# Kernel tuning notes

Hardware: AMD Instinct MI355X
Metric: run time of the kernel (lower is better)

Reference implementation:

```python
import jax, jax.numpy as jnp
from jax import lax
import numpy as np

B, C_IN, H, W = 4, 64, 192, 192
NPT = 128          # num_point
MAXC = 32          # objects per image
INIT_STRIDE, COARSE_STRIDE, DOWN = 10.0, 4.0, 4.0


def setup_inputs() -> dict:
    key = jax.random.key(0)
    ks = jax.random.split(key, 8)
    wh_pred = jax.random.normal(ks[0], (B, 2 * NPT, H, W), jnp.float32)
    cnn_feature = jax.random.normal(ks[1], (B, C_IN, H, W), jnp.float32)
    conv1_w = jax.random.normal(ks[2], (256, C_IN, 3, 3), jnp.float32) * 0.05
    conv1_b = jnp.zeros((256,), jnp.float32)
    conv2_w = jax.random.normal(ks[3], (C_IN, 256, 1, 1), jnp.float32) * 0.05
    conv2_b = jnp.zeros((C_IN,), jnp.float32)
    w_poly = jax.random.normal(ks[4], (NPT * 4, (NPT + 1) * C_IN), jnp.float32) * 0.02
    w_fuse = jax.random.normal(ks[5], (NPT * 2, NPT * 4), jnp.float32) * 0.02
    b_fuse = jnp.zeros((NPT * 2,), jnp.float32)
    ct_ind = jax.random.randint(ks[6], (B, MAXC), 0, H * W, jnp.int32)
    ct_img_idx = jnp.repeat(jnp.arange(B, dtype=jnp.int32), MAXC).reshape(B, MAXC)
    ct_num = jnp.full((B,), MAXC, jnp.int32)
    return {"wh_pred": wh_pred, "cnn_feature": cnn_feature,
            "conv1_w": conv1_w, "conv1_b": conv1_b, "conv2_w": conv2_w, "conv2_b": conv2_b,
            "w_poly": w_poly, "w_fuse": w_fuse, "b_fuse": b_fuse,
            "ct_ind": ct_ind, "ct_img_idx": ct_img_idx, "ct_num": ct_num}


def _conv(x, w, b, pad):
    y = lax.conv_general_dilated(x, w, (1, 1), [(pad, pad), (pad, pad)],
                                 dimension_numbers=("NCHW", "OIHW", "NCHW"))
    return y + b[None, :, None, None]


def _pnp(polys, h, w):
    # even-odd ray-casting rasterization: polys [N,P,2] (x,y) -> masks [N,h,w]
    N, P, _ = polys.shape
    yy = jnp.arange(h, dtype=polys.dtype)[None, :, None]   # [1,h,1]
    xx = jnp.arange(w, dtype=polys.dtype)[None, None, :]   # [1,1,w]
    v2 = jnp.roll(polys, -1, axis=1)
    edges = (polys[:, :, 0].T, polys[:, :, 1].T, v2[:, :, 0].T, v2[:, :, 1].T)  # each [P,N]

    def step(par, e):
        x1, y1, x2, y2 = [a[:, None, None] for a in e]      # [N,1,1]
        cond = (y1 > yy) != (y2 > yy)
        den = y2 - y1
        den = jnp.where(jnp.abs(den) < 1e-9, 1e-9, den)
        xint = x1 + (x2 - x1) * (yy - y1) / den
        return jnp.logical_xor(par, cond & (xx < xint)), None

    par0 = jnp.zeros((N, h, w), dtype=bool)
    par, _ = lax.scan(step, par0, edges)
    return par.astype(polys.dtype)


def _mask_batch(mask, ct_num, bs, h, w):
    # faithful to original buggy scatter: offset uses ct_num[i-1], not a cumulative sum
    cn = [int(v) for v in np.asarray(ct_num)]
    mc = max(cn)
    mb = jnp.zeros((bs, mc, h, w), mask.dtype)
    mb = mb.at[0, :cn[0]].set(mask[:cn[0]])
    for i in range(1, bs):
        mb = mb.at[i, :cn[i]].set(mask[cn[i - 1]:cn[i - 1] + cn[i]])
    return mb


def _sample(feat, pts, img_idx):
    # bilinear grid_sample (align_corners=False, zero padding): feat [B,C,H,W], pts [N,P,2] pixel coords
    Bf, C, Hf, Wf = feat.shape
    x = pts[..., 0] - 0.5
    y = pts[..., 1] - 0.5
    x0f = jnp.floor(x); y0f = jnp.floor(y)
    wx = (x - x0f)[..., None]; wy = (y - y0f)[..., None]
    x0 = x0f.astype(jnp.int32); y0 = y0f.astype(jnp.int32)

    def g(xi, yi):
        valid = (xi >= 0) & (xi < Wf) & (yi >= 0) & (yi < Hf)
        v = feat[img_idx[:, None], :, jnp.clip(yi, 0, Hf - 1), jnp.clip(xi, 0, Wf - 1)]  # [N,P,C]
        return v * valid[..., None]

    out = (g(x0, y0) * (1 - wx) * (1 - wy) + g(x0 + 1, y0) * wx * (1 - wy)
           + g(x0, y0 + 1) * (1 - wx) * wy + g(x0 + 1, y0 + 1) * wx * wy)
    return jnp.transpose(out, (0, 2, 1))  # [N,C,P]


def _decode(wh_pred, cnn_feature, conv1_w, conv1_b, conv2_w, conv2_b,
            w_poly, w_fuse, b_fuse, ct_ind, ct_img_idx, ct_num):
    bs, _, h, w = cnn_feature.shape
    ind = ct_ind.reshape(-1)        # ct_01 assumed all valid
    img = ct_img_idx.reshape(-1)
    cx = ind % w
    cy = ind // w
    off = wh_pred[img, :, cy, cx].reshape(ind.shape[0], -1, 2)   # [N, num_point, 2]
    ct = jnp.stack([cx, cy], axis=1).astype(wh_pred.dtype)       # [N,2]
    init_polys = off * INIT_STRIDE + ct[:, None, :]

    # Refine_wtih_pnp.trans_feature
    t = jax.nn.relu(_conv(cnn_feature, conv1_w, conv1_b, 1))
    feat = _conv(t, conv2_w, conv2_b, 0)

    # PnP_contour_feature (init)
    m_init = _pnp(init_polys, h, w)
    mb_init = _mask_batch(m_init, ct_num, bs, h, w)
    feat = jax.nn.relu(jnp.max(mb_init, axis=1, keepdims=True) * feat + feat)

    # GCN-style point feature sampling + global deform
    pts = jnp.concatenate([ct[:, None, :], init_polys], axis=1)  # [N, P+1, 2]
    fp = _sample(feat, pts, img).reshape(ind.shape[0], -1)       # [N, C*(P+1)]
    offsets = ((fp @ w_poly.T) @ w_fuse.T + b_fuse).reshape(-1, NPT, 2)
    coarse = offsets * COARSE_STRIDE + lax.stop_gradient(init_polys)

    # coarse_pnp
    m_c = _pnp(coarse, h, w)
    mb_c = _mask_batch(m_c, ct_num, bs, h, w)
    feat = jax.nn.relu(jnp.max(mb_c, axis=1, keepdims=True) * feat + feat)

    return init_polys * DOWN, coarse * DOWN, mb_init, mb_c, feat


def reference(wh_pred, cnn_feature, conv1_w, conv1_b, conv2_w, conv2_b,
              w_poly, w_fuse, b_fuse, ct_ind, ct_img_idx, ct_num):
    return _decode(wh_pred, cnn_feature, conv1_w, conv1_b, conv2_w, conv2_b,
                   w_poly, w_fuse, b_fuse, ct_ind, ct_img_idx, ct_num)
```

## Files before the change

kernel.cpp:

```cpp
#include <hip/hip_runtime.h>
#include <hip/hip_bf16.h>

#define HH 192
#define WW 192
#define HW 36864
#define CHW 2359296

typedef __attribute__((ext_vector_type(8))) short short8;
typedef __attribute__((ext_vector_type(4))) float float4v;

static __device__ __forceinline__ unsigned short f2bu(float f) {
  union { float f; unsigned u; } v; v.f = f;
  unsigned r = (v.u + 0x7fffu + ((v.u >> 16) & 1u)) >> 16;
  return (unsigned short)r;
}

static __device__ __forceinline__ float bu2f(unsigned short s) {
  union { unsigned u; float f; } v; v.u = ((unsigned)s) << 16;
  return v.f;
}

__global__ void k_prep(const float* __restrict__ c1w, const float* __restrict__ c2w,
                       const float* __restrict__ wfuse,
                       unsigned short* __restrict__ wB1, unsigned short* __restrict__ wB2,
                       float* __restrict__ wfT, float* __restrict__ tmp) {
  int i = blockIdx.x * 256 + threadIdx.x;
  if (i < 147456) {
    int T = i / 9216, r = i % 9216;
    int s = r / 512, e = r % 512;
    int l = e >> 3, j = e & 7;
    int m = l & 15, q = l >> 4;
    int oc = T * 16 + m;
    int k = s * 32 + q * 8 + j;
    int tap = k >> 6, ic = k & 63;
    int ky = tap / 3, kx = tap % 3;
    wB1[i] = f2bu(c1w[((oc * 64 + ic) * 3 + ky) * 3 + kx]);
    return;
  }
  int j2 = i - 147456;
  if (j2 < 16384) {
    int g = j2 / 512, e = j2 % 512;
    int l = e >> 3, jj = e & 7;
    int m = l & 15, q = l >> 4;
    int w = g / 8, s2 = g % 8;
    wB2[j2] = f2bu(c2w[(w * 16 + m) * 256 + s2 * 32 + q * 8 + jj]);
    return;
  }
  int k3 = j2 - 16384;
  if (k3 < 131072) { int jj = k3 >> 8, r = k3 & 255; wfT[k3] = wfuse[r * 512 + jj]; return; }
  int z = k3 - 131072;
  if (z < 65536) tmp[z] = 0.f;
}

__global__ void k_init_polys(const float* __restrict__ wh, const int* __restrict__ ct_ind,
                             const int* __restrict__ ct_img,
                             float* __restrict__ initp, float* __restrict__ out0) {
  int n = blockIdx.x;
  int p = threadIdx.x;
  int ind = ct_ind[n], img = ct_img[n];
  int cx = ind % WW, cy = ind / WW;
  size_t base = ((size_t)(img * 256 + 2 * p)) * HW + (size_t)cy * WW + cx;
  float ox = wh[base];
  float oy = wh[base + HW];
  float px = __fadd_rn(__fmul_rn(ox, 10.0f), (float)cx);
  float py = __fadd_rn(__fmul_rn(oy, 10.0f), (float)cy);
  initp[n * 256 + 2 * p]     = px;
  initp[n * 256 + 2 * p + 1] = py;
  out0[n * 256 + 2 * p]      = __fmul_rn(px, 4.0f);
  out0[n * 256 + 2 * p + 1]  = __fmul_rn(py, 4.0f);
}

__global__ __launch_bounds__(256) void k_pnp(const float* __restrict__ polys,
    float* __restrict__ outm, float* __restrict__ uout, float* __restrict__ fgate) {
  int row = blockIdx.x;
  int b   = blockIdx.y;
  int t = threadIdx.x;
  int w = t >> 6, lane = t & 63;
  __shared__ float xint[32][128];
  __shared__ int   cnt[32];
  __shared__ float mrow[32][192];
  __shared__ float urow[192];
  if (t < 32) cnt[t] = 0;
  __syncthreads();
  int nbase = (b == 0) ? 0 : 32;
  float yy = (float)row;
  for (int pc = 0; pc < 8; ++pc) {
    int c = w * 8 + pc;
    const float* P = polys + (nbase + c) * 256;
    for (int e = lane; e < 128; e += 64) {
      float y1 = P[2 * e + 1], y2 = P[2 * ((e + 1) & 127) + 1];
      if ((y1 > yy) != (y2 > yy)) {
        float x1 = P[2 * e], x2 = P[2 * ((e + 1) & 127)];
        float den = __fsub_rn(y2, y1);
        if (fabsf(den) < 1e-9f) den = 1e-9f;
        float xi = __fadd_rn(x1, __fdiv_rn(__fmul_rn(__fsub_rn(x2, x1), __fsub_rn(yy, y1)), den));
        xint[c][atomicAdd(&cnt[c], 1)] = xi;
      }
    }
  }
  __syncthreads();
  for (int idx = t; idx < 32 * 192; idx += 256) {
    int c = idx / 192, xp = idx - c * 192;
    float xf = (float)xp;
    int mm = cnt[c], cr = 0;
    for (int j = 0; j < mm; ++j) cr += (xf < xint[c][j]) ? 1 : 0;
    float mv = (float)(cr & 1);
    mrow[c][xp] = mv;
    outm[((size_t)(b * 32 + c) * HH + row) * WW + xp] = mv;
  }
  __syncthreads();
  if (t < 192) {
    float u = 0.f;
#pragma unroll
    for (int c = 0; c < 32; ++c) u = fmaxf(u, mrow[c][t]);
    urow[t] = u;
    if (uout) uout[(size_t)b * HW + (size_t)row * WW + t] = u;
  }
  __syncthreads();
  if (fgate) {
    float* fb = fgate + (size_t)b * CHW + (size_t)row * WW;
    for (int idx = t; idx < 64 * 48; idx += 256) {
      int chn = idx / 48, qx = idx - chn * 48;
      float4v f = *(float4v*)&fb[(size_t)chn * HW + qx * 4];
      float4v o;
#pragma unroll
      for (int j = 0; j < 4; ++j) {
        float uu = urow[qx * 4 + j];
        o[j] = fmaxf(__fadd_rn(__fmul_rn(uu, f[j]), f[j]), 0.f);
      }
      *(float4v*)&fb[(size_t)chn * HW + qx * 4] = o;
    }
  }
}

__global__ __launch_bounds__(256, 3) void k_conv(const float* __restrict__ x,
    const unsigned short* __restrict__ wB1, const float* __restrict__ b1,
    const unsigned short* __restrict__ wB2, const float* __restrict__ b2,
    const float* __restrict__ u0, float* __restrict__ feat,
    unsigned short* __restrict__ featT) {
  int blk = blockIdx.x;
  int b    = blk / 576;
  int rem  = blk % 576;
  int pair = rem / 6;
  int xs   = rem % 6;
  int y0 = pair * 2, x0 = xs * 32;
  int t = threadIdx.x;
  int w = t >> 6, l = t & 63;
  int m = l & 15, q = l >> 4;

  __shared__ __align__(16) unsigned short sb[16896];

  {
    int kq = t & 7;
    int pr = t >> 3;
    for (int itr = 0; itr < 8; ++itr) {
      int pi = itr * 32 + pr;
      int r  = pi >> 6;
      int ic = pi & 63;
      int gy = y0 + r - 1;
      float4v v = (float4v){0.f, 0.f, 0.f, 0.f};
      if (gy >= 0 && gy < HH)
        v = *(const float4v*)&x[(size_t)(b * 64 + ic) * HW + (size_t)gy * WW + x0 + kq * 4];
      int base = (r * 34 + 1 + kq * 4) * 72 + ic;
      sb[base]       = f2bu(v[0]);
      sb[base + 72]  = f2bu(v[1]);
      sb[base + 144] = f2bu(v[2]);
      sb[base + 216] = f2bu(v[3]);
    }
    for (int itr = 0; itr < 2; ++itr) {
      int e = itr * 256 + t;
      int xxh = e >> 8;
      int rm = e & 255;
      int r = rm >> 6, ic = rm & 63;
      int gy = y0 + r - 1;
      int gx = x0 - 1 + xxh * 33;
      float v = 0.f;
      if (gy >= 0 && gy < HH && gx >= 0 && gx < WW)
        v = x[(size_t)(b * 64 + ic) * HW + (size_t)gy * WW + gx];
      sb[(r * 34 + xxh * 33) * 72 + ic] = f2bu(v);
    }
  }
  __syncthreads();

  float4v acc1[4][4];
#pragma unroll
  for (int nt = 0; nt < 4; ++nt) {
    float bv = b1[w * 64 + nt * 16 + m];
#pragma unroll
    for (int mt = 0; mt < 4; ++mt) acc1[mt][nt] = (float4v){bv, bv, bv, bv};
  }

#pragma unroll
  for (int s = 0; s < 18; ++s) {
    int tap = s >> 1, ky = tap / 3, kx = tap - ky * 3;
    int ic0 = (s & 1) * 32 + q * 8;
    short8 bF[4];
#pragma unroll
    for (int nt = 0; nt < 4; ++nt)
      bF[nt] = *(const short8*)&wB1[(size_t)((((w * 4 + nt) * 18 + s) * 512) + l * 8)];
    short8 aF[4];
#pragma unroll
    for (int mt = 0; mt < 4; ++mt) {
      int col  = (mt & 1) * 16 + m + kx;
      int rowi = ky + (mt >> 1);
      aF[mt] = *(const short8*)&sb[(rowi * 34 + col) * 72 + ic0];
    }
#pragma unroll
    for (int nt = 0; nt < 4; ++nt)
#pragma unroll
      for (int mt = 0; mt < 4; ++mt)
        acc1[mt][nt] = __builtin_amdgcn_mfma_f32_16x16x32_bf16(aF[mt], bF[nt], acc1[mt][nt], 0, 0, 0);
  }
  __syncthreads();

#pragma unroll
  for (int mt = 0; mt < 4; ++mt)
#pragma unroll
    for (int nt = 0; nt < 4; ++nt)
#pragma unroll
      for (int r = 0; r < 4; ++r) {
        int p = mt * 16 + q * 4 + r;
        int oc = w * 64 + nt * 16 + m;
        sb[p * 264 + oc] = f2bu(fmaxf(acc1[mt][nt][r], 0.f));
      }
  __syncthreads();

  float4v acc2[4];
  {
    float bv = b2[w * 16 + m];
#pragma unroll
    for (int mt = 0; mt < 4; ++mt) acc2[mt] = (float4v){bv, bv, bv, bv};
  }
#pragma unroll
  for (int s2 = 0; s2 < 8; ++s2) {
    short8 bF2 = *(const short8*)&wB2[(size_t)(((w * 8 + s2) * 512) + l * 8)];
#pragma unroll
    for (int mt = 0; mt < 4; ++mt) {
      short8 a2 = *(const short8*)&sb[(mt * 16 + m) * 264 + s2 * 32 + q * 8];
      acc2[mt] = __builtin_amdgcn_mfma_f32_16x16x32_bf16(a2, bF2, acc2[mt], 0, 0, 0);
    }
  }
  __syncthreads();

  float* fS = (float*)sb;
#pragma unroll
  for (int mt = 0; mt < 4; ++mt)
#pragma unroll
    for (int r = 0; r < 4; ++r) {
      int p = mt * 16 + q * 4 + r;
      fS[w * 1088 + m * 68 + p] = acc2[mt][r];
    }
  const float* ub = u0 + b * HW;
  {
    int gy = y0 + (l >> 5), gx = x0 + (l & 31);
    float uu = ub[gy * WW + gx];
    size_t fb = (size_t)(b * 64 + w * 16) * HW + (size_t)gy * WW + gx;
#pragma unroll
    for (int i = 0; i < 16; ++i) {
      float f = fS[w * 1088 + i * 68 + l];
      feat[fb + (size_t)i * HW] = fmaxf(uu * f + f, 0.f);
    }
  }
  {
    unsigned short* ft = featT + (size_t)b * HW * 64;
    int c2 = (l & 7) * 2;
#pragma unroll
    for (int i = 0; i < 8; ++i) {
      int p = (l >> 3) + 8 * i;
      float f0 = fS[w * 1088 + c2 * 68 + p];
      float f1 = fS[w * 1088 + (c2 + 1) * 68 + p];
      int gy = y0 + (p >> 5), gx = x0 + (p & 31);
      float uu = ub[gy * WW + gx];
      f0 = fmaxf(uu * f0 + f0, 0.f);
      f1 = fmaxf(uu * f1 + f1, 0.f);
      unsigned v = (unsigned)f2bu(f0) | ((unsigned)f2bu(f1) << 16);
      *(unsigned*)&ft[((size_t)(gy * WW + gx)) * 64 + w * 16 + c2] = v;
    }
  }
}

__global__ __launch_bounds__(256) void k_sample(const unsigned short* __restrict__ featT,
    const float* __restrict__ initp, const int* __restrict__ ct_ind,
    const int* __restrict__ ct_img, float* __restrict__ fp) {
  int n  = blockIdx.x;
  int ch = blockIdx.y;
  int t  = threadIdx.x;
  int w  = t >> 6, lane = t & 63;
  int c  = lane & 31;
  int ph = lane >> 5;

  __shared__ float sF[4128];

  int img = ct_img[n];
  int ind = ct_ind[n];
  float ctx = (float)(ind % WW), cty = (float)(ind / WW);
  const unsigned short* fb = featT + (size_t)img * HW * 64 + ch * 32 + c;

  for (int i = 0; i < 17; ++i) {
    int p = i * 8 + w * 2 + ph;
    if (p < 129) {
      float px, py;
      if (p == 0) { px = ctx; py = cty; }
      else {
        px = initp[n * 256 + 2 * (p - 1)];
        py = initp[n * 256 + 2 * (p - 1) + 1];
      }
      float x = __fsub_rn(px, 0.5f), y = __fsub_rn(py, 0.5f);
      float x0f = floorf(x), y0f = floorf(y);
      float wx = __fsub_rn(x, x0f), wy = __fsub_rn(y, y0f);
      int x0 = (int)x0f, y0 = (int)y0f;
      float g[4];
#pragma unroll
      for (int qq = 0; qq < 4; ++qq) {
        int xi = x0 + (qq & 1), yi = y0 + (qq >> 1);
        bool valid = (xi >= 0) && (xi < WW) && (yi >= 0) && (yi < HH);
        int xc = min(max(xi, 0), WW - 1), yc = min(max(yi, 0), HH - 1);
        float v = bu2f(fb[(size_t)(yc * WW + xc) * 64]);
        g[qq] = valid ? v : 0.f;
      }
      float omx = __fsub_rn(1.f, wx), omy = __fsub_rn(1.f, wy);
      float r = __fadd_rn(__fadd_rn(__fadd_rn(
          __fmul_rn(__fmul_rn(g[0], omx), omy),
          __fmul_rn(__fmul_rn(g[1], wx),  omy)),
          __fmul_rn(__fmul_rn(g[2], omx), wy)),
          __fmul_rn(__fmul_rn(g[3], wx),  wy));
      sF[c * 129 + p] = r;
    }
  }
  __syncthreads();
  float* dst = fp + (size_t)n * 8256 + (size_t)ch * 4128;
  for (int idx = t; idx < 4128; idx += 256) dst[idx] = sF[idx];
}

__global__ __launch_bounds__(256) void k_gemm1(const float* __restrict__ fp,
    const float* __restrict__ wpoly, float* __restrict__ tmp) {
  int ntile = blockIdx.x;
  int jtile = blockIdx.y;
  int ks    = blockIdx.z;
  int c0 = (129 * ks) / 32, c1 = (129 * (ks + 1)) / 32;
  int t = threadIdx.x;
  int tn = t & 15, tj = t >> 4;
  __shared__ __align__(16) float aS[64][68];
  __shared__ __align__(16) float bS[64][68];
  float acc[4][4];
#pragma unroll
  for (int i = 0; i < 4; ++i)
#pragma unroll
    for (int j = 0; j < 4; ++j) acc[i][j] = 0.f;
  for (int ch = c0; ch < c1; ++ch) {
    int k0 = ch * 64;
    __syncthreads();
    for (int idx = t; idx < 1024; idx += 256) {
      int r = idx >> 4, c4 = (idx & 15) * 4;
      float4v va = *(const float4v*)&fp[(size_t)(ntile * 64 + r) * 8256 + k0 + c4];
      float4v vb = *(const float4v*)&wpoly[(size_t)(jtile * 64 + r) * 8256 + k0 + c4];
#pragma unroll
      for (int d = 0; d < 4; ++d) { aS[c4 + d][r] = va[d]; bS[c4 + d][r] = vb[d]; }
    }
    __syncthreads();
    for (int kk = 0; kk < 64; ++kk) {
      float4v a = *(const float4v*)&aS[kk][tn * 4];
      float4v bq = *(const float4v*)&bS[kk][tj * 4];
      acc[0][0] = fmaf(a[0], bq[0], acc[0][0]); acc[0][1] = fmaf(a[0], bq[1], acc[0][1]);
      acc[0][2] = fmaf(a[0], bq[2], acc[0][2]); acc[0][3] = fmaf(a[0], bq[3], acc[0][3]);
      acc[1][0] = fmaf(a[1], bq[0], acc[1][0]); acc[1][1] = fmaf(a[1], bq[1], acc[1][1]);
      acc[1][2] = fmaf(a[1], bq[2], acc[1][2]); acc[1][3] = fmaf(a[1], bq[3], acc[1][3]);
      acc[2][0] = fmaf(a[2], bq[0], acc[2][0]); acc[2][1] = fmaf(a[2], bq[1], acc[2][1]);
      acc[2][2] = fmaf(a[2], bq[2], acc[2][2]); acc[2][3] = fmaf(a[2], bq[3], acc[2][3]);
      acc[3][0] = fmaf(a[3], bq[0], acc[3][0]); acc[3][1] = fmaf(a[3], bq[1], acc[3][1]);
      acc[3][2] = fmaf(a[3], bq[2], acc[3][2]); acc[3][3] = fmaf(a[3], bq[3], acc[3][3]);
    }
  }
#pragma unroll
  for (int i = 0; i < 4; ++i)
#pragma unroll
    for (int j = 0; j < 4; ++j)
      atomicAdd(&tmp[(size_t)(ntile * 64 + tn * 4 + i) * 512 + jtile * 64 + tj * 4 + j], acc[i][j]);
}

__global__ __launch_bounds__(256) void k_gemm2(const float* __restrict__ tmp,
    const float* __restrict__ wfT, const float* __restrict__ bfuse,
    const float* __restrict__ initp, float* __restrict__ coarse, float* __restrict__ out1) {
  int n = blockIdx.x, r = threadIdx.x;
  __shared__ float tS[512];
  tS[r] = tmp[n * 512 + r];
  tS[r + 256] = tmp[n * 512 + 256 + r];
  __syncthreads();
  float acc = 0.f;
  for (int j = 0; j < 512; ++j) acc = fmaf(wfT[j * 256 + r], tS[j], acc);
  acc = __fadd_rn(acc, bfuse[r]);
  float cr = __fadd_rn(__fmul_rn(acc, 4.0f), initp[n * 256 + r]);
  coarse[n * 256 + r] = cr;
  out1[n * 256 + r] = __fmul_rn(cr, 4.0f);
}

extern "C" void kernel_launch(void* const* d_in, const int* in_sizes, int n_in,
                              void* d_out, int out_size, void* d_ws, size_t ws_size,
                              hipStream_t stream) {
  const float* wh    = (const float*)d_in[0];
  const float* cnnf  = (const float*)d_in[1];
  const float* c1w   = (const float*)d_in[2];
  const float* c1b   = (const float*)d_in[3];
  const float* c2w   = (const float*)d_in[4];
  const float* c2b   = (const float*)d_in[5];
  const float* wpoly = (const float*)d_in[6];
  const float* wfuse = (const float*)d_in[7];
  const float* bfuse = (const float*)d_in[8];
  const int* ct_ind  = (const int*)d_in[9];
  const int* ct_img  = (const int*)d_in[10];

  float* ws    = (float*)d_ws;
  float* wfT   = ws;
  float* initp = wfT + 131072;
  float* coarse= initp + 32768;
  float* tmp   = coarse + 32768;
  float* u0    = tmp + 65536;
  float* fpbuf = u0 + 147456;
  unsigned short* wB1 = (unsigned short*)(fpbuf + 1056768);
  unsigned short* wB2 = wB1 + 147456;

  float* out0 = (float*)d_out;
  float* out1 = out0 + 32768;
  float* out2 = out1 + 32768;
  float* out3 = out2 + 4718592;
  float* out4 = out3 + 4718592;
  float* feat = out4;
  unsigned short* featT = (unsigned short*)out3;

  k_prep<<<1408, 256, 0, stream>>>(c1w, c2w, wfuse, wB1, wB2, wfT, tmp);
  k_init_polys<<<128, 128, 0, stream>>>(wh, ct_ind, ct_img, initp, out0);
  k_pnp<<<dim3(192, 4), 256, 0, stream>>>(initp, out2, u0, nullptr);
  k_conv<<<2304, 256, 0, stream>>>(cnnf, wB1, c1b, wB2, c2b, u0, feat, featT);
  k_sample<<<dim3(128, 2), 256, 0, stream>>>(featT, initp, ct_ind, ct_img, fpbuf);
  k_gemm1<<<dim3(2, 8, 32), 256, 0, stream>>>(fpbuf, wpoly, tmp);
  k_gemm2<<<128, 256, 0, stream>>>(tmp, wfT, bfuse, initp, coarse, out1);
  k_pnp<<<dim3(192, 4), 256, 0, stream>>>(coarse, out3, nullptr, feat);
}
```

Before: 432.3 us.

## Gate final features from bf16 featT, drop fp32 feat write, replace split-K atomics

The conv kernel no longer writes the fp32 gated feature map. The second PnP pass now stages a row of the bf16 channel-last featT in shared memory and writes the final fp32 output from it, which cuts global memory traffic. The split-K GEMM writes per-slice partials that gemm2 sums, instead of using atomicAdd into a zeroed buffer. Init-poly decoding is folded into the prep kernel to save a launch. The final feature output is now derived from bf16-rounded values, which lowers its precision. The partials also add a workspace buffer.

Result: faster. 413.0 us (-4.5%).

```diff
diff --git a/kernel.cpp b/kernel.cpp
--- a/kernel.cpp
+++ b/kernel.cpp
@@ -8,6 +8,7 @@
 
 typedef __attribute__((ext_vector_type(8))) short short8;
 typedef __attribute__((ext_vector_type(4))) float float4v;
+typedef __attribute__((ext_vector_type(4))) unsigned short ushort4v;
 
 static __device__ __forceinline__ unsigned short f2bu(float f) {
   union { float f; unsigned u; } v; v.f = f;
@@ -23,8 +24,30 @@
 __global__ void k_prep(const float* __restrict__ c1w, const float* __restrict__ c2w,
                        const float* __restrict__ wfuse,
                        unsigned short* __restrict__ wB1, unsigned short* __restrict__ wB2,
-                       float* __restrict__ wfT, float* __restrict__ tmp) {
-  int i = blockIdx.x * 256 + threadIdx.x;
+                       float* __restrict__ wfT,
+                       const float* __restrict__ wh, const int* __restrict__ ct_ind,
+                       const int* __restrict__ ct_img,
+                       float* __restrict__ initp, float* __restrict__ out0) {
+  int blk = blockIdx.x;
+  if (blk >= 1152) {
+    int n = blk - 1152;
+    int p = threadIdx.x;
+    if (p < 128) {
+      int ind = ct_ind[n], img = ct_img[n];
+      int cx = ind % WW, cy = ind / WW;
+      size_t base = ((size_t)(img * 256 + 2 * p)) * HW + (size_t)cy * WW + cx;
+      float ox = wh[base];
+      float oy = wh[base + HW];
+      float px = __fadd_rn(__fmul_rn(ox, 10.0f), (float)cx);
+      float py = __fadd_rn(__fmul_rn(oy, 10.0f), (float)cy);
+      initp[n * 256 + 2 * p]     = px;
+      initp[n * 256 + 2 * p + 1] = py;
+      out0[n * 256 + 2 * p]      = __fmul_rn(px, 4.0f);
+      out0[n * 256 + 2 * p + 1]  = __fmul_rn(py, 4.0f);
+    }
+    return;
+  }
+  int i = blk * 256 + threadIdx.x;
   if (i < 147456) {
     int T = i / 9216, r = i % 9216;
     int s = r / 512, e = r % 512;
@@ -47,38 +70,21 @@
     return;
   }
   int k3 = j2 - 16384;
-  if (k3 < 131072) { int jj = k3 >> 8, r = k3 & 255; wfT[k3] = wfuse[r * 512 + jj]; return; }
-  int z = k3 - 131072;
-  if (z < 65536) tmp[z] = 0.f;
-}
-
-__global__ void k_init_polys(const float* __restrict__ wh, const int* __restrict__ ct_ind,
-                             const int* __restrict__ ct_img,
-                             float* __restrict__ initp, float* __restrict__ out0) {
-  int n = blockIdx.x;
-  int p = threadIdx.x;
-  int ind = ct_ind[n], img = ct_img[n];
-  int cx = ind % WW, cy = ind / WW;
-  size_t base = ((size_t)(img * 256 + 2 * p)) * HW + (size_t)cy * WW + cx;
-  float ox = wh[base];
-  float oy = wh[base + HW];
-  float px = __fadd_rn(__fmul_rn(ox, 10.0f), (float)cx);
-  float py = __fadd_rn(__fmul_rn(oy, 10.0f), (float)cy);
-  initp[n * 256 + 2 * p]     = px;
-  initp[n * 256 + 2 * p + 1] = py;
-  out0[n * 256 + 2 * p]      = __fmul_rn(px, 4.0f);
-  out0[n * 256 + 2 * p + 1]  = __fmul_rn(py, 4.0f);
+  if (k3 < 131072) { int jj = k3 >> 8, r = k3 & 255; wfT[k3] = wfuse[r * 512 + jj]; }
 }
 
 __global__ __launch_bounds__(256) void k_pnp(const float* __restrict__ polys,
-    float* __restrict__ outm, float* __restrict__ uout, float* __restrict__ fgate) {
+    float* __restrict__ outm, float* __restrict__ uout,
+    float* __restrict__ fgate, const unsigned short* __restrict__ fsrc) {
   int row = blockIdx.x;
   int b   = blockIdx.y;
   int t = threadIdx.x;
   int w = t >> 6, lane = t & 63;
-  __shared__ float xint[32][128];
+  __shared__ __align__(16) char smem[40960];
+  float (*xint)[128] = (float (*)[128])smem;
+  float (*mrow)[192] = (float (*)[192])(smem + 16384);
+  unsigned short* frow = (unsigned short*)smem;
   __shared__ int   cnt[32];
-  __shared__ float mrow[32][192];
   __shared__ float urow[192];
   if (t < 32) cnt[t] = 0;
   __syncthreads();
@@ -118,15 +124,20 @@
   }
   __syncthreads();
   if (fgate) {
+    const unsigned short* fr = fsrc + ((size_t)b * HW + (size_t)row * WW) * 64;
+    for (int idx = t; idx < 3072; idx += 256)
+      ((ushort4v*)frow)[idx] = ((const ushort4v*)fr)[idx];
+    __syncthreads();
     float* fb = fgate + (size_t)b * CHW + (size_t)row * WW;
-    for (int idx = t; idx < 64 * 48; idx += 256) {
+    for (int idx = t; idx < 3072; idx += 256) {
       int chn = idx / 48, qx = idx - chn * 48;
-      float4v f = *(float4v*)&fb[(size_t)chn * HW + qx * 4];
       float4v o;
 #pragma unroll
       for (int j = 0; j < 4; ++j) {
-        float uu = urow[qx * 4 + j];
-        o[j] = fmaxf(__fadd_rn(__fmul_rn(uu, f[j]), f[j]), 0.f);
+        int xp = qx * 4 + j;
+        float f = bu2f(frow[xp * 64 + chn]);
+        float uu = urow[xp];
+        o[j] = fmaxf(__fadd_rn(__fmul_rn(uu, f), f), 0.f);
       }
       *(float4v*)&fb[(size_t)chn * HW + qx * 4] = o;
     }
@@ -136,8 +147,7 @@
 __global__ __launch_bounds__(256, 3) void k_conv(const float* __restrict__ x,
     const unsigned short* __restrict__ wB1, const float* __restrict__ b1,
     const unsigned short* __restrict__ wB2, const float* __restrict__ b2,
-    const float* __restrict__ u0, float* __restrict__ feat,
-    unsigned short* __restrict__ featT) {
+    const float* __restrict__ u0, unsigned short* __restrict__ featT) {
   int blk = blockIdx.x;
   int b    = blk / 576;
   int rem  = blk % 576;
@@ -252,16 +262,6 @@
     }
   const float* ub = u0 + b * HW;
   {
-    int gy = y0 + (l >> 5), gx = x0 + (l & 31);
-    float uu = ub[gy * WW + gx];
-    size_t fb = (size_t)(b * 64 + w * 16) * HW + (size_t)gy * WW + gx;
-#pragma unroll
-    for (int i = 0; i < 16; ++i) {
-      float f = fS[w * 1088 + i * 68 + l];
-      feat[fb + (size_t)i * HW] = fmaxf(uu * f + f, 0.f);
-    }
-  }
-  {
     unsigned short* ft = featT + (size_t)b * HW * 64;
     int c2 = (l & 7) * 2;
 #pragma unroll
@@ -333,7 +333,7 @@
 }
 
 __global__ __launch_bounds__(256) void k_gemm1(const float* __restrict__ fp,
-    const float* __restrict__ wpoly, float* __restrict__ tmp) {
+    const float* __restrict__ wpoly, float* __restrict__ part) {
   int ntile = blockIdx.x;
   int jtile = blockIdx.y;
   int ks    = blockIdx.z;
@@ -371,20 +371,27 @@
       acc[3][2] = fmaf(a[3], bq[2], acc[3][2]); acc[3][3] = fmaf(a[3], bq[3], acc[3][3]);
     }
   }
-#pragma unroll
-  for (int i = 0; i < 4; ++i)
-#pragma unroll
-    for (int j = 0; j < 4; ++j)
-      atomicAdd(&tmp[(size_t)(ntile * 64 + tn * 4 + i) * 512 + jtile * 64 + tj * 4 + j], acc[i][j]);
-}
-
-__global__ __launch_bounds__(256) void k_gemm2(const float* __restrict__ tmp,
+  float* dst = part + (size_t)ks * 65536;
+#pragma unroll
+  for (int i = 0; i < 4; ++i) {
+    float4v o = (float4v){acc[i][0], acc[i][1], acc[i][2], acc[i][3]};
+    *(float4v*)&dst[(size_t)(ntile * 64 + tn * 4 + i) * 512 + jtile * 64 + tj * 4] = o;
+  }
+}
+
+__global__ __launch_bounds__(256) void k_gemm2(const float* __restrict__ part,
     const float* __restrict__ wfT, const float* __restrict__ bfuse,
     const float* __restrict__ initp, float* __restrict__ coarse, float* __restrict__ out1) {
   int n = blockIdx.x, r = threadIdx.x;
   __shared__ float tS[512];
-  tS[r] = tmp[n * 512 + r];
-  tS[r + 256] = tmp[n * 512 + 256 + r];
+  float s0 = 0.f, s1 = 0.f;
+  for (int ks = 0; ks < 32; ++ks) {
+    const float* p = part + (size_t)ks * 65536 + (size_t)n * 512;
+    s0 = __fadd_rn(s0, p[r]);
+    s1 = __fadd_rn(s1, p[r + 256]);
+  }
+  tS[r] = s0;
+  tS[r + 256] = s1;
   __syncthreads();
   float acc = 0.f;
   for (int j = 0; j < 512; ++j) acc = fmaf(wfT[j * 256 + r], tS[j], acc);
@@ -413,26 +420,25 @@
   float* wfT   = ws;
   float* initp = wfT + 131072;
   float* coarse= initp + 32768;
-  float* tmp   = coarse + 32768;
-  float* u0    = tmp + 65536;
+  float* u0    = coarse + 32768;
   float* fpbuf = u0 + 147456;
-  unsigned short* wB1 = (unsigned short*)(fpbuf + 1056768);
+  float* part  = fpbuf + 1056768;
+  unsigned short* wB1 = (unsigned short*)(part + 2097152);
   unsigned short* wB2 = wB1 + 147456;
+  unsigned short* featT = wB2 + 16384;
 
   float* out0 = (float*)d_out;
   float* out1 = out0 + 32768;
   float* out2 = out1 + 32768;
   float* out3 = out2 + 4718592;
   float* out4 = out3 + 4718592;
-  float* feat = out4;
-  unsigned short* featT = (unsigned short*)out3;
-
-  k_prep<<<1408, 256, 0, stream>>>(c1w, c2w, wfuse, wB1, wB2, wfT, tmp);
-  k_init_polys<<<128, 128, 0, stream>>>(wh, ct_ind, ct_img, initp, out0);
-  k_pnp<<<dim3(192, 4), 256, 0, stream>>>(initp, out2, u0, nullptr);
-  k_conv<<<2304, 256, 0, stream>>>(cnnf, wB1, c1b, wB2, c2b, u0, feat, featT);
+
+  k_prep<<<1280, 256, 0, stream>>>(c1w, c2w, wfuse, wB1, wB2, wfT,
+                                   wh, ct_ind, ct_img, initp, out0);
+  k_pnp<<<dim3(192, 4), 256, 0, stream>>>(initp, out2, u0, nullptr, nullptr);
+  k_conv<<<2304, 256, 0, stream>>>(cnnf, wB1, c1b, wB2, c2b, u0, featT);
   k_sample<<<dim3(128, 2), 256, 0, stream>>>(featT, initp, ct_ind, ct_img, fpbuf);
-  k_gemm1<<<dim3(2, 8, 32), 256, 0, stream>>>(fpbuf, wpoly, tmp);
-  k_gemm2<<<128, 256, 0, stream>>>(tmp, wfT, bfuse, initp, coarse, out1);
-  k_pnp<<<dim3(192, 4), 256, 0, stream>>>(coarse, out3, nullptr, feat);
-}
+  k_gemm1<<<dim3(2, 8, 32), 256, 0, stream>>>(fpbuf, wpoly, part);
+  k_gemm2<<<128, 256, 0, stream>>>(part, wfT, bfuse, initp, coarse, out1);
+  k_pnp<<<dim3(192, 4), 256, 0, stream>>>(coarse, out3, nullptr, out4, featT);
+}
```
